# Kernel optimization log

Hardware: AMD Instinct MI355X
Metric: run time of the kernel (lower is better)

The kernel has to match this reference:

```python
import jax, jax.numpy as jnp
import numpy as np

B, L, N, F = 8, 12, 1024, 3
H, ND, T, P, NL, GD = 32, 10, 10, 3, 2, 2
ALPHA, PROP = 3.0, 0.05
DOUT = (P + NL - 1) * H  # 128, forced by out_fc_in concat arithmetic


def setup_inputs() -> dict:
    key = jax.random.key(0)
    ks = iter(jax.random.split(key, 48))
    def g(shape, s=0.1):
        return jax.random.normal(next(ks), shape, jnp.float32) * s
    feats = jax.random.normal(next(ks), (B, L, N, F), jnp.float32)
    tid = jax.random.uniform(next(ks), (B, L, N, 1), jnp.float32, 0.0, 1.0 - 1e-4)
    diw = jax.random.randint(next(ks), (B, L, N, 1), 0, 7).astype(jnp.float32)
    history_data = jnp.concatenate([feats, tid, diw], axis=-1)
    return {
        'history_data': history_data,
        'W_emb': g((F, H)), 'b_emb': g((H,)),
        'T_emb': g((288, T)), 'D_emb': g((7, T)),
        'node_u': g((N, ND)), 'node_d': g((N, ND)),
        'W_std': g((P - 1, H + ND + 2 * T, H)), 'b_std': g((P - 1, H)),
        'W_mlp': g((P + 1, H, 1)), 'b_mlp': g((P + 1, 1)),
        'W_start': g((32, L)), 'b_start': g((32,)),
        'W_g': g((NL, H, H)),
        'W_rnn': g((H, DOUT)), 'b_rnn': g((DOUT,)),
        'W_e1': g((128, 32)), 'b_e1': g((128,)),
        'W_e2': g((L, 128)), 'b_e2': g((L,)),
        'M': g((N, DOUT), 1.0),
        'W_f1': g((2 * P * H + NL * H + 2 * T, 512)), 'b_f1': g((512,)),
        'W_f2': g((512, 3)), 'b_f2': g((3,)),
        'W_e3': g((4, L)), 'b_e3': g((4,)),
    }


def reference(history_data, W_emb, b_emb, T_emb, D_emb, node_u, node_d,
              W_std, b_std, W_mlp, b_mlp, W_start, b_start, W_g,
              W_rnn, b_rnn, W_e1, b_e1, W_e2, b_e2, M,
              W_f1, b_f1, W_f2, b_f2, W_e3, b_e3):
    feats = history_data[..., :F]
    tid_idx = (history_data[..., F] * 288).astype(jnp.int32)   # [B,L,N]
    diw_idx = history_data[..., F + 1].astype(jnp.int32)
    tid = T_emb[tid_idx]  # [B,L,N,T] gather
    diw = D_emb[diw_idx]
    hist = feats @ W_emb + b_emb  # [B,L,N,H] embedding

    # STD decomposition: gated filters peel off P-1 pattern components
    node_b = jnp.broadcast_to(node_u[None, None], (B, L, N, ND))
    xs, resid = [], hist
    for i in range(P - 1):
        inp = jnp.concatenate([hist, node_b, tid, diw], axis=-1)
        xi = jax.nn.sigmoid(inp @ W_std[i] + b_std[i]) * hist
        xs.append(xi)
        resid = resid - xi
    xs.append(resid)

    # Node_Clusterer (vectorized argmin routing + batch-mode)
    hist_mean = jnp.mean(hist @ W_mlp[0] + b_mlp[0], axis=1)  # [B,N,1]
    x_mean = jnp.concatenate(
        [jnp.mean(xs[p] @ W_mlp[p + 1] + b_mlp[p + 1], axis=1) for p in range(P)],
        axis=-1)  # [B,N,P]
    ratio = x_mean / (hist_mean + 1e-6)
    centers = jnp.max(ratio, axis=1, keepdims=True)  # [B,1,P]
    dist = jnp.abs(ratio - centers)
    assign = jnp.argmin(dist, axis=-1)  # [B,N]
    counts = jnp.sum(jax.nn.one_hot(assign, P, dtype=jnp.float32), axis=0)  # [N,P]
    label = jnp.argmax(counts, axis=-1)  # [N] mode over batch (ties -> smallest)
    masks = jax.nn.one_hot(label, P, dtype=jnp.float32).T  # [P,N]
    h0 = jnp.concatenate(xs, axis=-1)  # [B,L,N,P*H]

    # DSTGNN: learned directed adjacency
    m1, m2 = jnp.tanh(ALPHA * node_u), jnp.tanh(ALPHA * node_d)
    A = jax.nn.relu(jnp.tanh(ALPHA * (m1 @ m2.T - m2 @ m1.T)))  # [N,N]

    # SIE: per-pattern masked residual GCN on the clustered subgraphs
    x0 = jnp.einsum('cl,blnh->bcnh', W_start, hist) + b_start[None, :, None, None]
    out = jnp.zeros((B, 32, N, H), jnp.float32)
    for p in range(P):
        mp = masks[p]
        Ap = A * mp[:, None] * mp[None, :]
        Ap = Ap / (jnp.sum(Ap, axis=1, keepdims=True) + 1e-6)
        acc = jnp.zeros_like(x0)
        for l in range(NL):
            h = x0
            for _ in range(GD):
                h = PROP * x0 + (1.0 - PROP) * jnp.einsum('nm,bcmh->bcnh', Ap, h)
            acc = acc + jnp.einsum('bcnh,hk->bcnk', h, W_g[l])
        out = out + acc * mp[None, None, :, None]

    x_out = jnp.tanh(out @ W_rnn + b_rnn)  # [B,32,N,128]
    x_out = jax.nn.relu(jnp.einsum('oc,bcnh->bonh', W_e1, x_out) + b_e1[None, :, None, None])
    x_out = jnp.einsum('oc,bcnh->bonh', W_e2, x_out) + b_e2[None, :, None, None]  # [B,12,N,128]
    x_out = x_out * M[None, None]  # LearnableMatrixModel per-node scale

    fh = jnp.concatenate([x_out, hist, h0, tid, diw], axis=-1)  # [B,12,N,276]
    fc = jax.nn.relu(jax.nn.relu(fh) @ W_f1 + b_f1) @ W_f2 + b_f2  # [B,12,N,3]
    fc = jnp.einsum('oc,bcnh->bonh', W_e3, fc) + b_e3[None, :, None, None]  # [B,4,N,3]
    return jnp.transpose(fc, (0, 2, 1, 3)).reshape(B, N, -1)  # [B,N,12]
```

## Files before the change

kernel.cpp:

```cpp
#include <hip/hip_runtime.h>
#include <math.h>

#define BB 8
#define LL 12
#define NN 1024
#define FF 3
#define HH 32
#define NDD 10
#define TTT 10
#define PP 3
#define DOUTT 128
constexpr float kALPHA = 3.0f;

typedef __attribute__((ext_vector_type(8))) short short8v;
typedef __attribute__((ext_vector_type(4))) float float4v;

__device__ __forceinline__ unsigned short f2bf(float x) {
    union { float f; unsigned u; } v; v.f = x;
    unsigned r = v.u + 0x7FFF + ((v.u >> 16) & 1);
    return (unsigned short)(r >> 16);
}
__device__ __forceinline__ float bf2f(unsigned short u) {
    union { unsigned u; float f; } v; v.u = ((unsigned)u) << 16;
    return v.f;
}

__device__ __forceinline__ void gload_lds16(const unsigned short* g, unsigned short* l) {
    __builtin_amdgcn_global_load_lds(
        (const __attribute__((address_space(1))) void*)g,
        (__attribute__((address_space(3))) void*)l,
        16, 0, 0);
}

__device__ __forceinline__ void stage_tile(const unsigned short* __restrict__ g, int stride,
                                           unsigned short* tile, int tid) {
#pragma unroll
    for (int rr = 0; rr < 2; rr++) {
        int c = rr*256 + tid;
        int row = c >> 2;
        int q = (c & 3) ^ ((row >> 1) & 3);
        gload_lds16(g + (size_t)row*stride + q*8,
                    tile + ((size_t)(rr*256 + (tid & 192)))*8);
    }
}

__device__ __forceinline__ void stage_tileA512(const unsigned short* __restrict__ g, int stride,
                                               unsigned short* tile, int tid) {
    int row = tid >> 2;
    int q = (tid & 3) ^ ((row >> 1) & 3);
    gload_lds16(g + (size_t)row*stride + q*8,
                tile + ((size_t)(tid & ~63))*8);
}

__device__ __forceinline__ void stage_tileB512(const unsigned short* __restrict__ g, int stride,
                                               unsigned short* tile, int tid) {
#pragma unroll
    for (int rr = 0; rr < 4; rr++) {
        int c = rr*512 + tid;
        int row = c >> 2;
        int q = (c & 3) ^ ((row >> 1) & 3);
        gload_lds16(g + (size_t)row*stride + q*8,
                    tile + ((size_t)(rr*512 + (tid & ~63)))*8);
    }
}

constexpr size_t OFF_HIST    = 0;
constexpr size_t OFF_S4      = OFF_HIST   + (size_t)BB*LL*NN*HH;
constexpr size_t OFF_RATIO   = OFF_S4     + (size_t)BB*LL*NN*4;
constexpr size_t OFF_CENT    = OFF_RATIO  + (size_t)BB*NN*3;
constexpr size_t OFF_M1      = OFF_CENT   + 32;
constexpr size_t OFF_M2      = OFF_M1     + (size_t)NN*NDD;
constexpr size_t OFF_LABEL   = OFF_M2     + (size_t)NN*NDD;
constexpr size_t OFF_AN      = OFF_LABEL  + NN;
constexpr size_t OFF_ACOMBB  = OFF_AN     + (size_t)NN*NN;
constexpr size_t OFF_X0      = OFF_ACOMBB + (size_t)NN*NN/2;
constexpr size_t OFF_HFINB   = OFF_X0     + (size_t)NN*BB*HH*HH;
constexpr size_t OFF_WCOMBOT = OFF_HFINB  + (size_t)NN*BB*HH*HH/2;
constexpr size_t OFF_WE1B    = OFF_WCOMBOT+ 1024*4;
constexpr size_t OFF_FC      = OFF_WE1B   + 1024*4;
constexpr size_t OFF_ANB     = OFF_FC     + (size_t)BB*LL*NN*3;
constexpr size_t OFF_ANBT    = OFF_ANB    + (size_t)NN*NN/2;
constexpr size_t OFF_X0T     = OFF_ANBT   + (size_t)NN*NN/2;
constexpr size_t OFF_W1HI    = OFF_X0T    + (size_t)BB*HH*HH*NN/2;
constexpr size_t OFF_FHB     = OFF_W1HI   + (size_t)512*288/2;
constexpr size_t WS_FLOATS   = OFF_FHB    + (size_t)BB*LL*NN*288/2;

__global__ __launch_bounds__(256) void k1_embed(
    const float* __restrict__ hd, const float* __restrict__ W_emb, const float* __restrict__ b_emb,
    const float* __restrict__ T_emb, const float* __restrict__ D_emb, const float* __restrict__ node_u,
    const float* __restrict__ W_std, const float* __restrict__ b_std,
    const float* __restrict__ W_mlp, const float* __restrict__ b_mlp,
    float* __restrict__ hist, unsigned short* __restrict__ fhB, float* __restrict__ s4)
{
    __shared__ float sW[2*62*32];
    for (int i = threadIdx.x; i < 2*62*32; i += 256) sW[i] = W_std[i];
    __syncthreads();

    int pos = blockIdx.x*256 + threadIdx.x;
    int n = pos & (NN-1);
    const float* hp = hd + (size_t)pos*5;
    float f0 = hp[0], f1 = hp[1], f2 = hp[2];
    int ti = (int)(hp[3]*288.0f);
    int di = (int)hp[4];

    float tv[10], dv[10], nu[10];
#pragma unroll
    for (int t = 0; t < 10; t++) {
        tv[t] = T_emb[ti*10+t]; dv[t] = D_emb[di*10+t]; nu[t] = node_u[n*10+t];
    }
    float h[32];
#pragma unroll
    for (int j = 0; j < 32; j++) h[j] = b_emb[j] + f0*W_emb[j] + f1*W_emb[32+j] + f2*W_emb[64+j];

    float a0[32], a1[32];
#pragma unroll
    for (int j = 0; j < 32; j++) { a0[j] = b_std[j]; a1[j] = b_std[32+j]; }

    auto accum = [&](float v, int i) {
#pragma unroll
        for (int q = 0; q < 8; q++) {
            float4 w0 = *(const float4*)&sW[i*32 + q*4];
            float4 w1 = *(const float4*)&sW[(62+i)*32 + q*4];
            a0[q*4+0] += v*w0.x; a0[q*4+1] += v*w0.y; a0[q*4+2] += v*w0.z; a0[q*4+3] += v*w0.w;
            a1[q*4+0] += v*w1.x; a1[q*4+1] += v*w1.y; a1[q*4+2] += v*w1.z; a1[q*4+3] += v*w1.w;
        }
    };
#pragma unroll
    for (int i = 0; i < 32; i++) accum(h[i], i);
#pragma unroll
    for (int i = 0; i < 10; i++) accum(nu[i], 32+i);
#pragma unroll
    for (int i = 0; i < 10; i++) accum(tv[i], 42+i);
#pragma unroll
    for (int i = 0; i < 10; i++) accum(dv[i], 52+i);

    float x0v[32], x1v[32], rv[32];
    float s0 = b_mlp[0], s1 = b_mlp[1], s2 = b_mlp[2], s3 = b_mlp[3];
#pragma unroll
    for (int j = 0; j < 32; j++) {
        float sg0 = 1.f/(1.f + __expf(-a0[j]));
        float sg1 = 1.f/(1.f + __expf(-a1[j]));
        x0v[j] = sg0*h[j]; x1v[j] = sg1*h[j]; rv[j] = h[j] - x0v[j] - x1v[j];
        s0 += h[j]  * W_mlp[j];
        s1 += x0v[j]* W_mlp[32+j];
        s2 += x1v[j]* W_mlp[64+j];
        s3 += rv[j] * W_mlp[96+j];
    }
    float* ho = hist + (size_t)pos*32;
#pragma unroll
    for (int q = 0; q < 8; q++)
        *(float4*)&ho[q*4] = make_float4(h[q*4], h[q*4+1], h[q*4+2], h[q*4+3]);

    unsigned short* fr = fhB + (size_t)pos*288;
#pragma unroll
    for (int q = 0; q < 4; q++) {
        short8v v;
#pragma unroll
        for (int e = 0; e < 8; e++) v[e] = (short)f2bf(fmaxf(h[q*8+e], 0.f));
        *(short8v*)&fr[128 + q*8] = v;
    }
#pragma unroll
    for (int q = 0; q < 4; q++) {
        short8v v;
#pragma unroll
        for (int e = 0; e < 8; e++) v[e] = (short)f2bf(fmaxf(x0v[q*8+e], 0.f));
        *(short8v*)&fr[160 + q*8] = v;
    }
#pragma unroll
    for (int q = 0; q < 4; q++) {
        short8v v;
#pragma unroll
        for (int e = 0; e < 8; e++) v[e] = (short)f2bf(fmaxf(x1v[q*8+e], 0.f));
        *(short8v*)&fr[192 + q*8] = v;
    }
#pragma unroll
    for (int q = 0; q < 4; q++) {
        short8v v;
#pragma unroll
        for (int e = 0; e < 8; e++) v[e] = (short)f2bf(fmaxf(rv[q*8+e], 0.f));
        *(short8v*)&fr[224 + q*8] = v;
    }
    float tail[32];
#pragma unroll
    for (int i = 0; i < 32; i++) tail[i] = (i < 10) ? tv[i] : ((i < 20) ? dv[i-10] : 0.f);
#pragma unroll
    for (int q = 0; q < 4; q++) {
        short8v v;
#pragma unroll
        for (int e = 0; e < 8; e++) v[e] = (short)f2bf(fmaxf(tail[q*8+e], 0.f));
        *(short8v*)&fr[256 + q*8] = v;
    }
    *(float4*)&s4[(size_t)pos*4] = make_float4(s0, s1, s2, s3);
}

__global__ void k2_ratio(const float* __restrict__ s4, float* __restrict__ ratio)
{
    int bn = blockIdx.x*256 + threadIdx.x;
    if (bn >= BB*NN) return;
    int b = bn >> 10, n = bn & 1023;
    float a0=0, a1=0, a2=0, a3=0;
    for (int l = 0; l < 12; l++) {
        const float* sp = s4 + ((size_t)(b*12+l)*NN + n)*4;
        a0 += sp[0]; a1 += sp[1]; a2 += sp[2]; a3 += sp[3];
    }
    float hm = a0/12.f;
    float* rp = ratio + (size_t)bn*3;
    rp[0] = (a1/12.f)/(hm + 1e-6f);
    rp[1] = (a2/12.f)/(hm + 1e-6f);
    rp[2] = (a3/12.f)/(hm + 1e-6f);
}

__global__ __launch_bounds__(256) void k3_centers(const float* __restrict__ ratio, float* __restrict__ centers)
{
    int b = blockIdx.x;
    float m0=-3.4e38f, m1v=-3.4e38f, m2v=-3.4e38f;
    for (int n = threadIdx.x; n < NN; n += 256) {
        const float* rp = ratio + ((size_t)b*NN + n)*3;
        m0 = fmaxf(m0, rp[0]); m1v = fmaxf(m1v, rp[1]); m2v = fmaxf(m2v, rp[2]);
    }
#pragma unroll
    for (int off = 32; off > 0; off >>= 1) {
        m0  = fmaxf(m0,  __shfl_down(m0,  off));
        m1v = fmaxf(m1v, __shfl_down(m1v, off));
        m2v = fmaxf(m2v, __shfl_down(m2v, off));
    }
    __shared__ float red[4][3];
    int wid = threadIdx.x >> 6, lane = threadIdx.x & 63;
    if (lane == 0) { red[wid][0]=m0; red[wid][1]=m1v; red[wid][2]=m2v; }
    __syncthreads();
    if (threadIdx.x == 0) {
        centers[b*3+0] = fmaxf(fmaxf(red[0][0],red[1][0]), fmaxf(red[2][0],red[3][0]));
        centers[b*3+1] = fmaxf(fmaxf(red[0][1],red[1][1]), fmaxf(red[2][1],red[3][1]));
        centers[b*3+2] = fmaxf(fmaxf(red[0][2],red[1][2]), fmaxf(red[2][2],red[3][2]));
    }
}

__global__ void k4_labels(const float* __restrict__ ratio, const float* __restrict__ centers,
                          const float* __restrict__ node_u, const float* __restrict__ node_d,
                          int* __restrict__ label, float* __restrict__ m1, float* __restrict__ m2)
{
    int n = blockIdx.x*256 + threadIdx.x;
    if (n >= NN) return;
    int c0=0, c1=0, c2=0;
    for (int b = 0; b < BB; b++) {
        const float* rp = ratio + ((size_t)b*NN + n)*3;
        const float* cp = centers + b*3;
        float d0 = fabsf(rp[0]-cp[0]), d1 = fabsf(rp[1]-cp[1]), d2 = fabsf(rp[2]-cp[2]);
        int a = 0; float best = d0;
        if (d1 < best) { best = d1; a = 1; }
        if (d2 < best) { best = d2; a = 2; }
        if (a == 0) c0++; else if (a == 1) c1++; else c2++;
    }
    int lab = 0, bc = c0;
    if (c1 > bc) { bc = c1; lab = 1; }
    if (c2 > bc) { bc = c2; lab = 2; }
    label[n] = lab;
#pragma unroll
    for (int d = 0; d < 10; d++) {
        m1[n*10+d] = tanhf(kALPHA*node_u[n*10+d]);
        m2[n*10+d] = tanhf(kALPHA*node_d[n*10+d]);
    }
}

__global__ __launch_bounds__(256) void k5_A(const float* __restrict__ m1, const float* __restrict__ m2,
                                            const int* __restrict__ label, float* __restrict__ An)
{
    int n = blockIdx.x;
    __shared__ float row[1024];
    __shared__ float m1n[10], m2n[10];
    __shared__ float ssum[4];
    int t = threadIdx.x;
    if (t < 10) { m1n[t] = m1[n*10+t]; m2n[t] = m2[n*10+t]; }
    __syncthreads();
    int labn = label[n];
    float lsum = 0.f;
    for (int m = t; m < 1024; m += 256) {
        float a = 0.f;
        if (label[m] == labn) {
            float x = 0.f;
#pragma unroll
            for (int d = 0; d < 10; d++) x += m1n[d]*m2[m*10+d] - m2n[d]*m1[m*10+d];
            a = fmaxf(tanhf(3.f*x), 0.f);
        }
        row[m] = a; lsum += a;
    }
#pragma unroll
    for (int off = 32; off > 0; off >>= 1) lsum += __shfl_down(lsum, off);
    int wid = t >> 6, lane = t & 63;
    if (lane == 0) ssum[wid] = lsum;
    __syncthreads();
    float inv = 1.f/((ssum[0]+ssum[1]+ssum[2]+ssum[3]) + 1e-6f);
    for (int m = t; m < 1024; m += 256) An[(size_t)n*1024 + m] = row[m]*inv;
}

template<bool ALSO_DIRECT>
__global__ __launch_bounds__(256) void kt_transpose(const float* __restrict__ in,
                                                    unsigned short* __restrict__ outT,
                                                    unsigned short* __restrict__ outD,
                                                    int R, int C)
{
    __shared__ float tile[64][65];
    int c0 = blockIdx.x*64, r0 = blockIdx.y*64;
    for (int i = threadIdx.x; i < 64*64; i += 256) {
        int r = i >> 6, c = i & 63;
        float v = in[(size_t)(r0+r)*C + c0+c];
        tile[r][c] = v;
        if (ALSO_DIRECT) outD[(size_t)(r0+r)*C + c0+c] = f2bf(v);
    }
    __syncthreads();
    for (int i = threadIdx.x; i < 64*64; i += 256) {
        int c = i >> 6, r = i & 63;
        outT[(size_t)(c0+c)*R + r0+r] = f2bf(tile[r][c]);
    }
}

template<int MODE>
__global__ __launch_bounds__(256) void gemm_mfma(
    const unsigned short* __restrict__ A, const unsigned short* __restrict__ B,
    void* __restrict__ Cout, int Nout, int K)
{
    __shared__ __align__(16) unsigned short lds[2][2][2][128*32];
    const int t = threadIdx.x;

    int id = blockIdx.x + gridDim.x*blockIdx.y;
    int gx8 = gridDim.x >> 3;
    int xcd = id & 7, local = id >> 3;
    int bx = xcd*gx8 + (local % gx8);
    int by = local / gx8;

    const int lane = t & 63, wid = t >> 6;
    const int wr = wid >> 1, wc = wid & 1;
    const int l15 = lane & 15, l4 = lane >> 4;
    const int swq8 = (l4 ^ ((l15 >> 1) & 3))*8;
    const int row0 = by*128, col0 = bx*128;

    float4v acc[4][4];
#pragma unroll
    for (int i = 0; i < 4; i++)
#pragma unroll
        for (int j = 0; j < 4; j++) acc[i][j] = (float4v){0.f,0.f,0.f,0.f};

    const unsigned short* Ab = A + (size_t)row0*K;
    const unsigned short* Bb = B + (size_t)col0*K;

    stage_tile(Ab +  0, K, lds[0][0][0], t); stage_tile(Bb +  0, K, lds[0][1][0], t);
    stage_tile(Ab + 32, K, lds[0][0][1], t); stage_tile(Bb + 32, K, lds[0][1][1], t);
    __syncthreads();

    const int nk = K >> 6;
    for (int ks = 0; ks < nk; ks++) {
        int cur = ks & 1;
        if (ks + 1 < nk) {
            stage_tile(Ab + (ks+1)*64,      K, lds[cur^1][0][0], t);
            stage_tile(Bb + (ks+1)*64,      K, lds[cur^1][1][0], t);
            stage_tile(Ab + (ks+1)*64 + 32, K, lds[cur^1][0][1], t);
            stage_tile(Bb + (ks+1)*64 + 32, K, lds[cur^1][1][1], t);
        }
#pragma unroll
        for (int kk = 0; kk < 2; kk++) {
            short8v a[4], b[4];
#pragma unroll
            for (int f = 0; f < 4; f++) {
                a[f] = *(const short8v*)&lds[cur][0][kk][(wr*64 + f*16 + l15)*32 + swq8];
                b[f] = *(const short8v*)&lds[cur][1][kk][(wc*64 + f*16 + l15)*32 + swq8];
            }
#pragma unroll
            for (int i = 0; i < 4; i++)
#pragma unroll
                for (int j = 0; j < 4; j++)
                    acc[i][j] = __builtin_amdgcn_mfma_f32_16x16x32_bf16(a[i], b[j], acc[i][j], 0, 0, 0);
        }
        __syncthreads();
    }

#pragma unroll
    for (int i = 0; i < 4; i++) {
#pragma unroll
        for (int j = 0; j < 4; j++) {
            int gc = col0 + wc*64 + j*16 + l15;
#pragma unroll
            for (int r = 0; r < 4; r++) {
                int gr = row0 + wr*64 + i*16 + l4*4 + r;
                if (MODE == 0) {
                    float an = bf2f(A[(size_t)gr*K + gc]);
                    float v = 0.9025f*acc[i][j][r] + 0.0475f*an + ((gr==gc) ? 0.05f : 0.f);
                    ((unsigned short*)Cout)[(size_t)gr*Nout + gc] = f2bf(v);
                } else {
                    ((unsigned short*)Cout)[(size_t)gr*Nout + gc] = f2bf(acc[i][j][r]);
                }
            }
        }
    }
}

__global__ __launch_bounds__(256) void k7_x0(const float* __restrict__ hist,
                                             const float* __restrict__ W_start, const float* __restrict__ b_start,
                                             float* __restrict__ x0)
{
    int bid = blockIdx.x; int n = bid & (NN-1), b = bid >> 10;
    __shared__ float hl[384];
    __shared__ float sw[384];
    int t = threadIdx.x;
    for (int idx = t; idx < 384; idx += 256) {
        int l = idx >> 5, hh = idx & 31;
        hl[idx] = hist[((size_t)(b*12+l)*NN + n)*32 + hh];
    }
    for (int idx = t; idx < 384; idx += 256) sw[idx] = W_start[idx];
    __syncthreads();
    int c = t >> 3, h4 = (t & 7)*4;
    float bs = b_start[c];
    float o0 = bs, o1 = bs, o2 = bs, o3 = bs;
#pragma unroll
    for (int l = 0; l < 12; l++) {
        float w = sw[c*12+l];
        o0 += w*hl[l*32+h4];   o1 += w*hl[l*32+h4+1];
        o2 += w*hl[l*32+h4+2]; o3 += w*hl[l*32+h4+3];
    }
    *(float4*)&x0[(size_t)n*8192 + b*1024 + c*32 + h4] = make_float4(o0, o1, o2, o3);
}

__global__ void kw_combo2(const float* __restrict__ W_g, const float* __restrict__ W_rnn,
                          const float* __restrict__ W_e1,
                          unsigned short* __restrict__ wcomboT, unsigned short* __restrict__ we1B)
{
    int j = threadIdx.x;
    for (int hh = 0; hh < 32; hh++) {
        float s = 0.f;
        for (int k = 0; k < 32; k++) s += (W_g[hh*32+k] + W_g[1024 + hh*32+k]) * W_rnn[k*128 + j];
        wcomboT[j*32 + hh] = f2bf(s);
    }
    for (int i = j; i < 4096; i += 128) we1B[i] = f2bf(W_e1[i]);
}

__global__ __launch_bounds__(256) void k9_mfma(
    const unsigned short* __restrict__ hfinB,
    const unsigned short* __restrict__ wcomboT,
    const float* __restrict__ b_rnn,
    const unsigned short* __restrict__ we1B,
    const float* __restrict__ b_e1,
    const float* __restrict__ W_e2,
    const float* __restrict__ b_e2,
    const float* __restrict__ Mm,
    unsigned short* __restrict__ fhB)
{
    __shared__ __align__(16) unsigned short xrT[4][1024];
    __shared__ float sWe2T[128][12];
    __shared__ float sBe1[128];
    __shared__ float sBe2[16];

    const int t = threadIdx.x;
    const int bid = blockIdx.x;
    const int n = bid & (NN-1), b = bid >> 10;
    const int lane = t & 63, wid = t >> 6;
    const int l15 = lane & 15, l4 = lane >> 4;
    const int j0 = wid*32;

    for (int i = t; i < 12*128; i += 256) {
        int o2 = i >> 7, o1 = i & 127;
        sWe2T[o1][o2] = W_e2[i];
    }
    if (t < 128) sBe1[t] = b_e1[t];
    if (t < 12)  sBe2[t] = b_e2[t];
    __syncthreads();

    const unsigned short* Hb = hfinB + (size_t)n*8192 + (size_t)b*1024;
    short8v ah[2], bw[2];
#pragma unroll
    for (int f = 0; f < 2; f++) {
        ah[f] = *(const short8v*)&Hb[(f*16 + l15)*32 + l4*8];
        bw[f] = *(const short8v*)&wcomboT[(j0 + f*16 + l15)*32 + l4*8];
    }
    float br[2];
    br[0] = b_rnn[j0 + l15];
    br[1] = b_rnn[j0 + 16 + l15];
    float4v accA[2][2];
#pragma unroll
    for (int cf = 0; cf < 2; cf++)
#pragma unroll
        for (int jf = 0; jf < 2; jf++)
            accA[cf][jf] = (float4v){br[jf], br[jf], br[jf], br[jf]};
#pragma unroll
    for (int cf = 0; cf < 2; cf++)
#pragma unroll
        for (int jf = 0; jf < 2; jf++)
            accA[cf][jf] = __builtin_amdgcn_mfma_f32_16x16x32_bf16(ah[cf], bw[jf], accA[cf][jf], 0, 0, 0);

#pragma unroll
    for (int cf = 0; cf < 2; cf++)
#pragma unroll
        for (int jf = 0; jf < 2; jf++) {
            int jl = jf*16 + l15;
            int csw = (cf*16 + l4*4) ^ ((jl & 3) << 3);
            unsigned short p0 = f2bf(tanhf(accA[cf][jf][0]));
            unsigned short p1 = f2bf(tanhf(accA[cf][jf][1]));
            unsigned short p2 = f2bf(tanhf(accA[cf][jf][2]));
            unsigned short p3 = f2bf(tanhf(accA[cf][jf][3]));
            unsigned int lo = (unsigned)p0 | ((unsigned)p1 << 16);
            unsigned int hi = (unsigned)p2 | ((unsigned)p3 << 16);
            *(uint2*)&xrT[wid][jl*32 + csw] = make_uint2(lo, hi);
        }

    short8v bx[2];
#pragma unroll
    for (int jf = 0; jf < 2; jf++) {
        int jl = jf*16 + l15;
        int csw = (l4*8) ^ ((jl & 3) << 3);
        bx[jf] = *(const short8v*)&xrT[wid][jl*32 + csw];
    }
    float4v accB[8][2];
#pragma unroll
    for (int of = 0; of < 8; of++)
#pragma unroll
        for (int jf = 0; jf < 2; jf++) accB[of][jf] = (float4v){0.f,0.f,0.f,0.f};
#pragma unroll
    for (int of = 0; of < 8; of++) {
        short8v aw = *(const short8v*)&we1B[(of*16 + l15)*32 + l4*8];
        accB[of][0] = __builtin_amdgcn_mfma_f32_16x16x32_bf16(aw, bx[0], accB[of][0], 0, 0, 0);
        accB[of][1] = __builtin_amdgcn_mfma_f32_16x16x32_bf16(aw, bx[1], accB[of][1], 0, 0, 0);
    }

    float v0[12], v1[12];
#pragma unroll
    for (int o2 = 0; o2 < 12; o2++) { v0[o2] = 0.f; v1[o2] = 0.f; }
#pragma unroll
    for (int of = 0; of < 8; of++) {
#pragma unroll
        for (int r = 0; r < 4; r++) {
            int o1 = of*16 + l4*4 + r;
            float be = sBe1[o1];
            float z0 = fmaxf(accB[of][0][r] + be, 0.f);
            float z1 = fmaxf(accB[of][1][r] + be, 0.f);
#pragma unroll
            for (int q = 0; q < 3; q++) {
                float4 w = *(const float4*)&sWe2T[o1][q*4];
                v0[q*4+0] += w.x*z0; v0[q*4+1] += w.y*z0; v0[q*4+2] += w.z*z0; v0[q*4+3] += w.w*z0;
                v1[q*4+0] += w.x*z1; v1[q*4+1] += w.y*z1; v1[q*4+2] += w.z*z1; v1[q*4+3] += w.w*z1;
            }
        }
    }
#pragma unroll
    for (int o2 = 0; o2 < 12; o2++) {
        v0[o2] += __shfl_xor(v0[o2], 16);
        v0[o2] += __shfl_xor(v0[o2], 32);
        v1[o2] += __shfl_xor(v1[o2], 16);
        v1[o2] += __shfl_xor(v1[o2], 32);
    }

    float mm0 = Mm[(size_t)n*128 + j0 + l15];
    float mm1 = Mm[(size_t)n*128 + j0 + 16 + l15];
#pragma unroll
    for (int e = 0; e < 3; e++) {
        int o2 = l4*3 + e;
        float be2 = sBe2[o2];
        size_t base = ((size_t)((b*12 + o2)*NN + n))*288;
        float val0 = (v0[o2] + be2) * mm0;
        float val1 = (v1[o2] + be2) * mm1;
        fhB[base + j0 + l15]      = f2bf(fmaxf(val0, 0.f));
        fhB[base + j0 + 16 + l15] = f2bf(fmaxf(val1, 0.f));
    }
}

__global__ void kt_w1(const float* __restrict__ W_f1, unsigned short* __restrict__ w1hi)
{
    int idx = blockIdx.x*256 + threadIdx.x;
    if (idx >= 512*288) return;
    int n = idx / 288, k = idx - n*288;
    float w = (k < 276) ? W_f1[(size_t)k*512 + n] : 0.f;
    w1hi[idx] = f2bf(w);
}

__global__ __launch_bounds__(512, 2) void k10_mfma2(
    const unsigned short* __restrict__ fhB, const unsigned short* __restrict__ w1hi,
    const float* __restrict__ b_f1, const float* __restrict__ W_f2, float* __restrict__ fc)
{
    __shared__ __align__(16) unsigned short smem[40960];
    unsigned short (*Abuf)[128*32]  = (unsigned short(*)[128*32])smem;
    unsigned short (*Bhbuf)[512*32] = (unsigned short(*)[512*32])(smem + 8192);
    float* fcp = (float*)smem;

    const int t = threadIdx.x;
    int id = blockIdx.x;
    int by = (id & 7)*96 + (id >> 3);
    const int pos0 = by*128;

    const int lane = t & 63, w = t >> 6;
    const int wr = w >> 2, wc = w & 3;
    const int l15 = lane & 15, l4 = lane >> 4;
    const int swq8 = (l4 ^ ((l15 >> 1) & 3))*8;

    float4v acc[4][8];
#pragma unroll
    for (int i = 0; i < 4; i++)
#pragma unroll
        for (int j = 0; j < 8; j++) acc[i][j] = (float4v){0.f,0.f,0.f,0.f};

    const unsigned short* Ab = fhB + (size_t)pos0*288;

    stage_tileA512(Ab,   288, Abuf[0],  t);
    stage_tileB512(w1hi, 288, Bhbuf[0], t);
    __syncthreads();

    for (int ks = 0; ks < 9; ks++) {
        int cur = ks & 1;
        if (ks + 1 < 9) {
            stage_tileA512(Ab   + (ks+1)*32, 288, Abuf[cur^1],  t);
            stage_tileB512(w1hi + (ks+1)*32, 288, Bhbuf[cur^1], t);
        }
        short8v a[4];
#pragma unroll
        for (int f = 0; f < 4; f++)
            a[f] = *(const short8v*)&Abuf[cur][(wr*64 + f*16 + l15)*32 + swq8];
#pragma unroll
        for (int j = 0; j < 8; j++) {
            int brow = wc*128 + j*16 + l15;
            short8v bh = *(const short8v*)&Bhbuf[cur][brow*32 + swq8];
#pragma unroll
            for (int i = 0; i < 4; i++)
                acc[i][j] = __builtin_amdgcn_mfma_f32_16x16x32_bf16(a[i], bh, acc[i][j], 0, 0, 0);
        }
        __syncthreads();
    }

    for (int i = t; i < 384; i += 512) fcp[i] = 0.f;
    __syncthreads();

    float pk[4][4][3];
#pragma unroll
    for (int i = 0; i < 4; i++)
#pragma unroll
        for (int r = 0; r < 4; r++)
#pragma unroll
            for (int k = 0; k < 3; k++) pk[i][r][k] = 0.f;

#pragma unroll
    for (int j = 0; j < 8; j++) {
        int gc = wc*128 + j*16 + l15;
        float bias = b_f1[gc];
        float w20 = W_f2[gc*3+0], w21 = W_f2[gc*3+1], w22 = W_f2[gc*3+2];
#pragma unroll
        for (int i = 0; i < 4; i++)
#pragma unroll
            for (int r = 0; r < 4; r++) {
                float z = fmaxf(acc[i][j][r] + bias, 0.f);
                pk[i][r][0] += z*w20; pk[i][r][1] += z*w21; pk[i][r][2] += z*w22;
            }
    }
#pragma unroll
    for (int i = 0; i < 4; i++)
#pragma unroll
        for (int r = 0; r < 4; r++) {
            int rowL = wr*64 + i*16 + l4*4 + r;
            atomicAdd(&fcp[rowL*3 + 0], pk[i][r][0]);
            atomicAdd(&fcp[rowL*3 + 1], pk[i][r][1]);
            atomicAdd(&fcp[rowL*3 + 2], pk[i][r][2]);
        }
    __syncthreads();
    for (int i = t; i < 384; i += 512) {
        fc[(size_t)pos0*3 + i] = fcp[i];
    }
}

__global__ void k11_e3(const float* __restrict__ fc, const float* __restrict__ b_f2,
                       const float* __restrict__ W_e3, const float* __restrict__ b_e3,
                       float* __restrict__ out)
{
    int idx = blockIdx.x*256 + threadIdx.x;
    if (idx >= BB*NN*12) return;
    int ok = idx % 12;
    int o = ok / 3, k = ok % 3;
    int bn = idx / 12;
    int n = bn & 1023, b = bn >> 10;
    float s = b_e3[o];
    float bk = b_f2[k];
#pragma unroll
    for (int c = 0; c < 12; c++)
        s += W_e3[o*12+c] * (fc[((size_t)(b*12+c)*NN + n)*3 + k] + bk);
    out[idx] = s;
}

extern "C" void kernel_launch(void* const* d_in, const int* in_sizes, int n_in,
                              void* d_out, int out_size, void* d_ws, size_t ws_size,
                              hipStream_t stream)
{
    const float* hd      = (const float*)d_in[0];
    const float* W_emb   = (const float*)d_in[1];
    const float* b_emb   = (const float*)d_in[2];
    const float* T_emb   = (const float*)d_in[3];
    const float* D_emb   = (const float*)d_in[4];
    const float* node_u  = (const float*)d_in[5];
    const float* node_d  = (const float*)d_in[6];
    const float* W_std   = (const float*)d_in[7];
    const float* b_std   = (const float*)d_in[8];
    const float* W_mlp   = (const float*)d_in[9];
    const float* b_mlp   = (const float*)d_in[10];
    const float* W_start = (const float*)d_in[11];
    const float* b_start = (const float*)d_in[12];
    const float* W_g     = (const float*)d_in[13];
    const float* W_rnn   = (const float*)d_in[14];
    const float* b_rnn   = (const float*)d_in[15];
    const float* W_e1    = (const float*)d_in[16];
    const float* b_e1    = (const float*)d_in[17];
    const float* W_e2    = (const float*)d_in[18];
    const float* b_e2    = (const float*)d_in[19];
    const float* Mm      = (const float*)d_in[20];
    const float* W_f1    = (const float*)d_in[21];
    const float* b_f1    = (const float*)d_in[22];
    const float* W_f2    = (const float*)d_in[23];
    const float* b_f2    = (const float*)d_in[24];
    const float* W_e3    = (const float*)d_in[25];
    const float* b_e3    = (const float*)d_in[26];

    float* ws      = (float*)d_ws;
    float* hist    = ws + OFF_HIST;
    float* s4      = ws + OFF_S4;
    float* ratio   = ws + OFF_RATIO;
    float* cent    = ws + OFF_CENT;
    float* m1      = ws + OFF_M1;
    float* m2      = ws + OFF_M2;
    int*   label   = (int*)(ws + OFF_LABEL);
    float* An      = ws + OFF_AN;
    unsigned short* AcombB  = (unsigned short*)(ws + OFF_ACOMBB);
    float* x0      = ws + OFF_X0;
    unsigned short* hfinB   = (unsigned short*)(ws + OFF_HFINB);
    unsigned short* wcomboT = (unsigned short*)(ws + OFF_WCOMBOT);
    unsigned short* we1B    = (unsigned short*)(ws + OFF_WE1B);
    float* fc      = ws + OFF_FC;
    unsigned short* AnB   = (unsigned short*)(ws + OFF_ANB);
    unsigned short* AnBT  = (unsigned short*)(ws + OFF_ANBT);
    unsigned short* x0T   = (unsigned short*)(ws + OFF_X0T);
    unsigned short* w1hi  = (unsigned short*)(ws + OFF_W1HI);
    unsigned short* fhB   = (unsigned short*)(ws + OFF_FHB);

    k1_embed<<<(BB*LL*NN)/256, 256, 0, stream>>>(hd, W_emb, b_emb, T_emb, D_emb, node_u,
                                                 W_std, b_std, W_mlp, b_mlp, hist, fhB, s4);
    k2_ratio<<<(BB*NN)/256, 256, 0, stream>>>(s4, ratio);
    k3_centers<<<BB, 256, 0, stream>>>(ratio, cent);
    k4_labels<<<NN/256, 256, 0, stream>>>(ratio, cent, node_u, node_d, label, m1, m2);
    k5_A<<<NN, 256, 0, stream>>>(m1, m2, label, An);
    kt_transpose<true><<<dim3(16, 16), 256, 0, stream>>>(An, AnBT, AnB, 1024, 1024);
    gemm_mfma<0><<<dim3(8, 8), 256, 0, stream>>>(AnB, AnBT, AcombB, 1024, 1024);
    k7_x0<<<BB*NN, 256, 0, stream>>>(hist, W_start, b_start, x0);
    kt_transpose<false><<<dim3(128, 16), 256, 0, stream>>>(x0, x0T, (unsigned short*)0, 1024, 8192);
    gemm_mfma<2><<<dim3(64, 8), 256, 0, stream>>>(AcombB, x0T, hfinB, 8192, 1024);
    kw_combo2<<<1, 128, 0, stream>>>(W_g, W_rnn, W_e1, wcomboT, we1B);
    k9_mfma<<<BB*NN, 256, 0, stream>>>(hfinB, wcomboT, b_rnn, we1B, b_e1, W_e2, b_e2, Mm, fhB);
    kt_w1<<<(512*288)/256, 256, 0, stream>>>(W_f1, w1hi);
    k10_mfma2<<<768, 512, 0, stream>>>(fhB, w1hi, b_f1, W_f2, fc);
    k11_e3<<<(BB*NN*12)/256, 256, 0, stream>>>(fc, b_f2, W_e3, b_e3, (float*)d_out);
}
```

Before: 398.5 us.

## Make FC1 kernel weight-stationary with resident W_f1 column slices and atomic reduction

The fused FC1+FC2 kernel is restructured so each block keeps a 128-column slice of W_f1 resident in LDS across 12 row tiles, instead of restaging the full 512-column weight for every 128-row tile. Each of 256 blocks (4 slices × 64 row groups) reduces its partial FC2 outputs into global memory with atomicAdd, so the output buffer is now zeroed with a memset beforehand. The aim is to cut repeated weight staging traffic. In exchange the kernel loses double-buffered pipelining because each tile is loaded fully and then synchronised, adds global atomics and makes the float summation order non-deterministic.

```diff
diff --git a/kernel.cpp b/kernel.cpp
--- a/kernel.cpp
+++ b/kernel.cpp
@@ -50,18 +50,6 @@
     int q = (tid & 3) ^ ((row >> 1) & 3);
     gload_lds16(g + (size_t)row*stride + q*8,
                 tile + ((size_t)(tid & ~63))*8);
-}
-
-__device__ __forceinline__ void stage_tileB512(const unsigned short* __restrict__ g, int stride,
-                                               unsigned short* tile, int tid) {
-#pragma unroll
-    for (int rr = 0; rr < 4; rr++) {
-        int c = rr*512 + tid;
-        int row = c >> 2;
-        int q = (c & 3) ^ ((row >> 1) & 3);
-        gload_lds16(g + (size_t)row*stride + q*8,
-                    tile + ((size_t)(rr*512 + (tid & ~63)))*8);
-    }
 }
 
 constexpr size_t OFF_HIST    = 0;
@@ -569,94 +557,95 @@
     w1hi[idx] = f2bf(w);
 }
 
-__global__ __launch_bounds__(512, 2) void k10_mfma2(
+__global__ __launch_bounds__(512, 2) void k10_res(
     const unsigned short* __restrict__ fhB, const unsigned short* __restrict__ w1hi,
     const float* __restrict__ b_f1, const float* __restrict__ W_f2, float* __restrict__ fc)
 {
-    __shared__ __align__(16) unsigned short smem[40960];
-    unsigned short (*Abuf)[128*32]  = (unsigned short(*)[128*32])smem;
-    unsigned short (*Bhbuf)[512*32] = (unsigned short(*)[512*32])(smem + 8192);
-    float* fcp = (float*)smem;
+    __shared__ __align__(16) unsigned short Bres[9][128*32];
+    __shared__ __align__(16) unsigned short Abuf[9][128*32];
+    __shared__ float fcp[384];
 
     const int t = threadIdx.x;
-    int id = blockIdx.x;
-    int by = (id & 7)*96 + (id >> 3);
-    const int pos0 = by*128;
+    const int slice = blockIdx.x >> 6;
+    const int rg    = blockIdx.x & 63;
+    const int col0 = slice*128;
 
     const int lane = t & 63, w = t >> 6;
     const int wr = w >> 2, wc = w & 3;
     const int l15 = lane & 15, l4 = lane >> 4;
     const int swq8 = (l4 ^ ((l15 >> 1) & 3))*8;
 
-    float4v acc[4][8];
-#pragma unroll
-    for (int i = 0; i < 4; i++)
-#pragma unroll
-        for (int j = 0; j < 8; j++) acc[i][j] = (float4v){0.f,0.f,0.f,0.f};
-
-    const unsigned short* Ab = fhB + (size_t)pos0*288;
-
-    stage_tileA512(Ab,   288, Abuf[0],  t);
-    stage_tileB512(w1hi, 288, Bhbuf[0], t);
-    __syncthreads();
-
-    for (int ks = 0; ks < 9; ks++) {
-        int cur = ks & 1;
-        if (ks + 1 < 9) {
-            stage_tileA512(Ab   + (ks+1)*32, 288, Abuf[cur^1],  t);
-            stage_tileB512(w1hi + (ks+1)*32, 288, Bhbuf[cur^1], t);
+#pragma unroll
+    for (int ks = 0; ks < 9; ks++)
+        stage_tileA512(w1hi + (size_t)col0*288 + ks*32, 288, Bres[ks], t);
+
+    float bias[2], w2c[2][3];
+#pragma unroll
+    for (int j = 0; j < 2; j++) {
+        int gc = col0 + wc*32 + j*16 + l15;
+        bias[j] = b_f1[gc];
+        w2c[j][0] = W_f2[gc*3+0]; w2c[j][1] = W_f2[gc*3+1]; w2c[j][2] = W_f2[gc*3+2];
+    }
+
+    for (int s = 0; s < 12; s++) {
+        const int pos0 = (rg*12 + s)*128;
+        const unsigned short* Ab = fhB + (size_t)pos0*288;
+#pragma unroll
+        for (int ks = 0; ks < 9; ks++)
+            stage_tileA512(Ab + ks*32, 288, Abuf[ks], t);
+        if (t < 384) fcp[t] = 0.f;
+        __syncthreads();
+
+        float4v acc[4][2];
+#pragma unroll
+        for (int i = 0; i < 4; i++)
+#pragma unroll
+            for (int j = 0; j < 2; j++) acc[i][j] = (float4v){0.f,0.f,0.f,0.f};
+
+#pragma unroll
+        for (int ks = 0; ks < 9; ks++) {
+            short8v a[4], b[2];
+#pragma unroll
+            for (int f = 0; f < 4; f++)
+                a[f] = *(const short8v*)&Abuf[ks][(wr*64 + f*16 + l15)*32 + swq8];
+#pragma unroll
+            for (int j = 0; j < 2; j++)
+                b[j] = *(const short8v*)&Bres[ks][(wc*32 + j*16 + l15)*32 + swq8];
+#pragma unroll
+            for (int i = 0; i < 4; i++)
+#pragma unroll
+                for (int j = 0; j < 2; j++)
+                    acc[i][j] = __builtin_amdgcn_mfma_f32_16x16x32_bf16(a[i], b[j], acc[i][j], 0, 0, 0);
         }
-        short8v a[4];
-#pragma unroll
-        for (int f = 0; f < 4; f++)
-            a[f] = *(const short8v*)&Abuf[cur][(wr*64 + f*16 + l15)*32 + swq8];
-#pragma unroll
-        for (int j = 0; j < 8; j++) {
-            int brow = wc*128 + j*16 + l15;
-            short8v bh = *(const short8v*)&Bhbuf[cur][brow*32 + swq8];
+
+        float pk[4][4][3];
+#pragma unroll
+        for (int i = 0; i < 4; i++)
+#pragma unroll
+            for (int r = 0; r < 4; r++)
+#pragma unroll
+                for (int k = 0; k < 3; k++) pk[i][r][k] = 0.f;
+#pragma unroll
+        for (int j = 0; j < 2; j++)
 #pragma unroll
             for (int i = 0; i < 4; i++)
-                acc[i][j] = __builtin_amdgcn_mfma_f32_16x16x32_bf16(a[i], bh, acc[i][j], 0, 0, 0);
-        }
+#pragma unroll
+                for (int r = 0; r < 4; r++) {
+                    float z = fmaxf(acc[i][j][r] + bias[j], 0.f);
+                    pk[i][r][0] += z*w2c[j][0]; pk[i][r][1] += z*w2c[j][1]; pk[i][r][2] += z*w2c[j][2];
+                }
+#pragma unroll
+        for (int i = 0; i < 4; i++)
+#pragma unroll
+            for (int r = 0; r < 4; r++) {
+                int rowL = wr*64 + i*16 + l4*4 + r;
+                atomicAdd(&fcp[rowL*3 + 0], pk[i][r][0]);
+                atomicAdd(&fcp[rowL*3 + 1], pk[i][r][1]);
+                atomicAdd(&fcp[rowL*3 + 2], pk[i][r][2]);
+            }
         __syncthreads();
-    }
-
-    for (int i = t; i < 384; i += 512) fcp[i] = 0.f;
-    __syncthreads();
-
-    float pk[4][4][3];
-#pragma unroll
-    for (int i = 0; i < 4; i++)
-#pragma unroll
-        for (int r = 0; r < 4; r++)
-#pragma unroll
-            for (int k = 0; k < 3; k++) pk[i][r][k] = 0.f;
-
-#pragma unroll
-    for (int j = 0; j < 8; j++) {
-        int gc = wc*128 + j*16 + l15;
-        float bias = b_f1[gc];
-        float w20 = W_f2[gc*3+0], w21 = W_f2[gc*3+1], w22 = W_f2[gc*3+2];
-#pragma unroll
-        for (int i = 0; i < 4; i++)
-#pragma unroll
-            for (int r = 0; r < 4; r++) {
-                float z = fmaxf(acc[i][j][r] + bias, 0.f);
-                pk[i][r][0] += z*w20; pk[i][r][1] += z*w21; pk[i][r][2] += z*w22;
-            }
-    }
-#pragma unroll
-    for (int i = 0; i < 4; i++)
-#pragma unroll
-        for (int r = 0; r < 4; r++) {
-            int rowL = wr*64 + i*16 + l4*4 + r;
-            atomicAdd(&fcp[rowL*3 + 0], pk[i][r][0]);
-            atomicAdd(&fcp[rowL*3 + 1], pk[i][r][1]);
-            atomicAdd(&fcp[rowL*3 + 2], pk[i][r][2]);
-        }
-    __syncthreads();
-    for (int i = t; i < 384; i += 512) {
-        fc[(size_t)pos0*3 + i] = fcp[i];
+        if (t < 384) atomicAdd(&fc[(size_t)pos0*3 + t], fcp[t]);
+        __syncthreads();
     }
 }
 
@@ -745,6 +734,7 @@
     kw_combo2<<<1, 128, 0, stream>>>(W_g, W_rnn, W_e1, wcomboT, we1B);
     k9_mfma<<<BB*NN, 256, 0, stream>>>(hfinB, wcomboT, b_rnn, we1B, b_e1, W_e2, b_e2, Mm, fhB);
     kt_w1<<<(512*288)/256, 256, 0, stream>>>(W_f1, w1hi);
-    k10_mfma2<<<768, 512, 0, stream>>>(fhB, w1hi, b_f1, W_f2, fc);
+    hipMemsetAsync(fc, 0, (size_t)BB*LL*NN*3*sizeof(float), stream);
+    k10_res<<<256, 512, 0, stream>>>(fhB, w1hi, b_f1, W_f2, fc);
     k11_e3<<<(BB*NN*12)/256, 256, 0, stream>>>(fc, b_f2, W_e3, b_e3, (float*)d_out);
 }
```

Measured after the change: 764.5 us. 91.8% more time.
